# Kernel optimization log

Measured on AMD Instinct MI355X. Metric: run time of the kernel, lower is better.

The kernel has to match this reference:

```python
import jax, jax.numpy as jnp
import numpy as np

N_NODES = 50000
N_EDGES = 600000
D_IN = 128
HIDDEN = 128
N_CLASSES = 2
BN_EPS = 1e-5


def setup_inputs() -> dict:
    key = jax.random.key(0)
    ks = jax.random.split(key, 10)
    x = jax.random.normal(ks[0], (N_NODES, D_IN), dtype=jnp.float32)
    edge_index = jax.random.randint(ks[1], (2, N_EDGES), 0, N_NODES, dtype=jnp.int64)
    # weights stored [in, out] (transpose of torch Linear.weight)
    s1 = 1.0 / np.sqrt(D_IN)
    s2 = 1.0 / np.sqrt(HIDDEN)
    W1 = jax.random.uniform(ks[2], (D_IN, HIDDEN), jnp.float32, -s1, s1)
    b1 = jax.random.uniform(ks[3], (HIDDEN,), jnp.float32, -s1, s1)
    gamma = jnp.ones((HIDDEN,), jnp.float32)
    beta = jnp.zeros((HIDDEN,), jnp.float32)
    W2 = jax.random.uniform(ks[4], (HIDDEN, HIDDEN), jnp.float32, -s2, s2)
    b2 = jax.random.uniform(ks[5], (HIDDEN,), jnp.float32, -s2, s2)
    Wl = jax.random.uniform(ks[6], (HIDDEN, N_CLASSES), jnp.float32, -s2, s2)
    bl = jax.random.uniform(ks[7], (N_CLASSES,), jnp.float32, -s2, s2)
    return {"x": x, "edge_index": edge_index, "W1": W1, "b1": b1,
            "gamma": gamma, "beta": beta, "W2": W2, "b2": b2,
            "Wl": Wl, "bl": bl}


def reference(x, edge_index, W1, b1, gamma, beta, W2, b2, Wl, bl):
    src, dst = edge_index[0], edge_index[1]
    # GINConv with eps=0 (PyG default): h_i = MLP(x_i + sum_{j->i} x_j)
    agg = jax.ops.segment_sum(x[src], dst, num_segments=N_NODES)  # [N, D]
    h = x + agg
    # MLP: Linear -> ReLU -> BatchNorm1d (train-mode batch stats) -> Linear
    h = jax.nn.relu(h @ W1 + b1)
    mean = jnp.mean(h, axis=0)
    var = jnp.var(h, axis=0)
    h = (h - mean) * jax.lax.rsqrt(var + BN_EPS) * gamma + beta
    h = h @ W2 + b2
    # classifier head
    return h @ Wl + bl  # [N, num_classes]
```

## Files before the change

kernel.cpp:

```cpp
#include <hip/hip_runtime.h>
#include <cstdint>

#define NN 50000
#define NE 600000
#define D 128
#define NWAVE 3125
#define NBLK 782
#define BS 48
#define NB 196
#define PCAP 4608
#define FA 147
#define WB1 16
#define XB4 782
#define NREP 16

typedef __attribute__((ext_vector_type(8))) short short8;
typedef __attribute__((ext_vector_type(4))) float f32x4;

static __device__ __forceinline__ unsigned short f2bf(float f) {
  unsigned int u = __float_as_uint(f);
  unsigned int r = (u + 0x7FFFu + ((u >> 16) & 1u)) >> 16;
  return (unsigned short)r;
}

__global__ __launch_bounds__(256) void k_prep(const float* __restrict__ x,
                                              const float* __restrict__ W1,
                                              const float* __restrict__ W2,
                                              const float* __restrict__ Wl,
                                              const float* __restrict__ b2,
                                              const float* __restrict__ bl,
                                              const int* __restrict__ ei,
                                              unsigned short* __restrict__ xb,
                                              unsigned short* __restrict__ W1p,
                                              float* __restrict__ Cf,
                                              float* __restrict__ KBf,
                                              int* __restrict__ gcnt,
                                              unsigned* __restrict__ pairs) {
  __shared__ int histA[NB], baseA[NB], curA[NB];
  int blk = blockIdx.x, t = threadIdx.x;
  if (blk < FA) {
    if (t < NB) histA[t] = 0;
    __syncthreads();
    int e0 = blk * 4096 + t;
#pragma unroll
    for (int i = 0; i < 16; ++i) {
      int e = e0 + i * 256;
      if (e < NE) atomicAdd(&histA[ei[NE + e] >> 8], 1);
    }
    __syncthreads();
    if (t < NB) {
      int h = histA[t];
      baseA[t] = h ? atomicAdd(&gcnt[t], h) : 0;
      curA[t] = 0;
    }
    __syncthreads();
#pragma unroll
    for (int i = 0; i < 16; ++i) {
      int e = e0 + i * 256;
      if (e < NE) {
        int s = ei[e];
        int d = ei[NE + e];
        int b = d >> 8;
        int p = baseA[b] + atomicAdd(&curA[b], 1);
        if (p < PCAP) pairs[b * PCAP + p] = (unsigned)s | ((unsigned)(d & 255) << 16);
      }
    }
    return;
  }
  blk -= FA;
  if (blk < WB1) {
    int base = blk * 1024 + t;
#pragma unroll
    for (int i = 0; i < 4; ++i) {
      int rem = base + i * 256;
      int ks = rem >> 12;
      int nf = (rem >> 9) & 7;
      int l  = (rem >> 3) & 63;
      int j  = rem & 7;
      int k = ks * 32 + (l >> 4) * 8 + j;
      int n = nf * 16 + (l & 15);
      W1p[rem] = f2bf(W1[k * D + n]);
    }
    return;
  }
  blk -= WB1;
  if (blk == 0) {
    {
      int k = t >> 1, c = t & 1;
      const float4* w2r = (const float4*)(W2 + k * D);
      float s = 0.f;
#pragma unroll
      for (int m4 = 0; m4 < 32; ++m4) {
        float4 wv = w2r[m4];
        int m = m4 * 4;
        s += wv.x * Wl[(m + 0) * 2 + c] + wv.y * Wl[(m + 1) * 2 + c] +
             wv.z * Wl[(m + 2) * 2 + c] + wv.w * Wl[(m + 3) * 2 + c];
      }
      Cf[k * 2 + c] = s;
    }
    if (t < 2) {
      float s = bl[t];
      for (int m = 0; m < D; ++m) s += b2[m] * Wl[m * 2 + t];
      KBf[t] = s;
    }
    return;
  }
  blk -= 1;
  {
    int64_t base = (int64_t)blk * 1024 + t;
    const float4* xs = (const float4*)x;
#pragma unroll
    for (int i = 0; i < 4; ++i) {
      int64_t idx = base + i * 256;
      if (idx < (int64_t)NN * D / 8) {
        float4 f0 = xs[idx * 2], f1 = xs[idx * 2 + 1];
        uint4 o;
        o.x = (unsigned)f2bf(f0.x) | ((unsigned)f2bf(f0.y) << 16);
        o.y = (unsigned)f2bf(f0.z) | ((unsigned)f2bf(f0.w) << 16);
        o.z = (unsigned)f2bf(f1.x) | ((unsigned)f2bf(f1.y) << 16);
        o.w = (unsigned)f2bf(f1.z) | ((unsigned)f2bf(f1.w) << 16);
        ((uint4*)xb)[idx] = o;
      }
    }
  }
}

__global__ __launch_bounds__(256) void k_fusedA(const unsigned short* __restrict__ xb,
                                                const int* __restrict__ gcnt,
                                                const unsigned* __restrict__ pairs,
                                                const unsigned short* __restrict__ W1p,
                                                const float* __restrict__ b1,
                                                unsigned short* __restrict__ h1b,
                                                float* __restrict__ stats) {
  __shared__ uint4 tile[64 * 16];
  __shared__ unsigned short cs[64 * BS];
  __shared__ int cur[64];
  __shared__ float redS[D], redQ[D];
  int t = threadIdx.x;
  if (t < D) { redS[t] = 0.f; redQ[t] = 0.f; }
  if (t < 64) cur[t] = 0;
  __syncthreads();

  {
    int bkt = blockIdx.x >> 2, qt = blockIdx.x & 3;
    int cnt = gcnt[bkt]; if (cnt > PCAP) cnt = PCAP;
    for (int i = t; i < cnt; i += 256) {
      unsigned u = pairs[bkt * PCAP + i];
      int dloc = (u >> 16) & 255;
      if ((dloc >> 6) == qt) {
        int dl = dloc & 63;
        int pos = atomicAdd(&cur[dl], 1);
        if (pos < BS - 1) cs[dl * BS + pos] = (unsigned short)(u & 0xFFFFu);
      }
    }
  }
  __syncthreads();

  int w = t >> 6, lane = t & 63;
  int g = lane >> 4, l = lane & 15;
  int wave_id = blockIdx.x * 4 + w;
  bool valid = wave_id < NWAVE;
  int row0 = wave_id * 16;
  const uint4* xv = (const uint4*)xb;

  if (valid) {
#define GSRC(k) __shfl(((k) < 16 ? cl0 : ((k) < 32 ? cl1 : cl2)), (g << 4) + ((k) & 15))
#define MSK(v, kk) { unsigned m_ = ((kk) < dcap) ? 0xFFFFFFFFu : 0u; \
                     (v).x &= m_; (v).y &= m_; (v).z &= m_; (v).w &= m_; }
#define ACC8(v)                                     \
  { a0 += __uint_as_float((v).x << 16);             \
    a1 += __uint_as_float((v).x & 0xFFFF0000u);     \
    a2 += __uint_as_float((v).y << 16);             \
    a3 += __uint_as_float((v).y & 0xFFFF0000u);     \
    a4 += __uint_as_float((v).z << 16);             \
    a5 += __uint_as_float((v).z & 0xFFFF0000u);     \
    a6 += __uint_as_float((v).w << 16);             \
    a7 += __uint_as_float((v).w & 0xFFFF0000u); }
    for (int sub = 0; sub < 4; ++sub) {
      int dl = (w << 4) + (sub << 2) + g;
      int node = blockIdx.x * 64 + dl;
      int ec = cur[dl];
      if (ec > BS - 1) ec = BS - 1;
      int dcap = ec + 1;
      int cbase = dl * BS;
      int cl0 = (l < ec) ? (int)cs[cbase + l]
                         : ((l == ec) ? node : 0);
      int cl1 = (l + 16 < ec) ? (int)cs[cbase + 16 + l]
                              : ((l + 16 == ec) ? node : 0);
      int cl2 = (l + 32 < ec) ? (int)cs[cbase + 32 + l]
                              : ((l + 32 == ec) ? node : 0);
      int maxd = dcap;
      maxd = max(maxd, __shfl_xor(maxd, 16));
      maxd = max(maxd, __shfl_xor(maxd, 32));
      float a0 = 0, a1 = 0, a2 = 0, a3 = 0, a4 = 0, a5 = 0, a6 = 0, a7 = 0;
      int nit = (maxd + 7) >> 3;
      for (int it = 0; it < nit; ++it) {
        int k0 = it << 3;
        int i0 = GSRC(k0);
        int i1 = GSRC(k0 + 1);
        int i2 = GSRC(k0 + 2);
        int i3 = GSRC(k0 + 3);
        int i4 = GSRC(k0 + 4);
        int i5 = GSRC(k0 + 5);
        int i6 = GSRC(k0 + 6);
        int i7 = GSRC(k0 + 7);
        uint4 v0 = xv[(unsigned)i0 * 16u + l];
        uint4 v1 = xv[(unsigned)i1 * 16u + l];
        uint4 v2 = xv[(unsigned)i2 * 16u + l];
        uint4 v3 = xv[(unsigned)i3 * 16u + l];
        uint4 v4 = xv[(unsigned)i4 * 16u + l];
        uint4 v5 = xv[(unsigned)i5 * 16u + l];
        uint4 v6 = xv[(unsigned)i6 * 16u + l];
        uint4 v7 = xv[(unsigned)i7 * 16u + l];
        MSK(v0, k0) MSK(v1, k0 + 1) MSK(v2, k0 + 2) MSK(v3, k0 + 3)
        MSK(v4, k0 + 4) MSK(v5, k0 + 5) MSK(v6, k0 + 6) MSK(v7, k0 + 7)
        ACC8(v0) ACC8(v1) ACC8(v2) ACC8(v3)
        ACC8(v4) ACC8(v5) ACC8(v6) ACC8(v7)
      }
      uint4 o;
      o.x = (unsigned)f2bf(a0) | ((unsigned)f2bf(a1) << 16);
      o.y = (unsigned)f2bf(a2) | ((unsigned)f2bf(a3) << 16);
      o.z = (unsigned)f2bf(a4) | ((unsigned)f2bf(a5) << 16);
      o.w = (unsigned)f2bf(a6) | ((unsigned)f2bf(a7) << 16);
      tile[(dl * 16 + l) ^ (dl & 7)] = o;
    }
#undef GSRC
#undef MSK
#undef ACC8

    {
      int rb = (w << 4) + l;
      short8 a[4];
#pragma unroll
      for (int ks = 0; ks < 4; ++ks)
        a[ks] = *(const short8*)&tile[(rb * 16 + ks * 4 + g) ^ (rb & 7)];

      f32x4 acc[8];
#pragma unroll
      for (int nf = 0; nf < 8; ++nf) { f32x4 z = {0.f, 0.f, 0.f, 0.f}; acc[nf] = z; }

      const short8* B = (const short8*)W1p;
#pragma unroll
      for (int ks = 0; ks < 4; ++ks)
#pragma unroll
        for (int nf = 0; nf < 8; ++nf)
          acc[nf] = __builtin_amdgcn_mfma_f32_16x16x32_bf16(a[ks], B[(ks * 8 + nf) * 64 + lane],
                                                            acc[nf], 0, 0, 0);

#pragma unroll
      for (int nf = 0; nf < 8; ++nf) {
        int colc = nf * 16 + l;
        float bias = b1[colc];
        float ps = 0.f, pq = 0.f;
#pragma unroll
        for (int r = 0; r < 4; ++r) {
          float v = fmaxf(acc[nf][r] + bias, 0.f);
          int row = row0 + g * 4 + r;
          h1b[(int64_t)row * D + colc] = f2bf(v);
          ps += v; pq += v * v;
        }
        ps += __shfl_xor(ps, 16); ps += __shfl_xor(ps, 32);
        pq += __shfl_xor(pq, 16); pq += __shfl_xor(pq, 32);
        if (g == 0) { atomicAdd(&redS[colc], ps); atomicAdd(&redQ[colc], pq); }
      }
    }
  }
  __syncthreads();
  {
    int r = blockIdx.x & (NREP - 1);
    if (t < D) {
      unsafeAtomicAdd(&stats[r * 256 + t], redS[t]);
      unsafeAtomicAdd(&stats[r * 256 + D + t], redQ[t]);
    }
  }
}

__global__ __launch_bounds__(256) void k_head(const unsigned short* __restrict__ h1b,
                                              const float* __restrict__ stats,
                                              const float* __restrict__ gamma,
                                              const float* __restrict__ beta,
                                              const float* __restrict__ Cf,
                                              const float* __restrict__ KBf,
                                              float* __restrict__ out) {
  __shared__ float sc_s[D], sh_s[D];
  __shared__ float2 c2_s[D];
  int t = threadIdx.x;
  if (t < D) {
    float s = 0.f, q = 0.f;
#pragma unroll
    for (int r = 0; r < NREP; ++r) {
      s += stats[r * 256 + t];
      q += stats[r * 256 + D + t];
    }
    const float inv_n = 1.0f / (float)NN;
    float mean = s * inv_n;
    float var = q * inv_n - mean * mean;
    float sc = gamma[t] * rsqrtf(var + 1e-5f);
    sc_s[t] = sc;
    sh_s[t] = beta[t] - mean * sc;
    c2_s[t] = ((const float2*)Cf)[t];
  }
  __syncthreads();
  float2 kb = ((const float2*)KBf)[0];
  int l = t & 15;
  int k0 = l * 8;
#pragma unroll
  for (int rd = 0; rd < 4; ++rd) {
    int node = blockIdx.x * 64 + rd * 16 + (t >> 4);
    if (node < NN) {
      uint4 v = ((const uint4*)h1b)[(int64_t)node * 16 + l];
      float e0 = __uint_as_float(v.x << 16), e1 = __uint_as_float(v.x & 0xFFFF0000u);
      float e2 = __uint_as_float(v.y << 16), e3 = __uint_as_float(v.y & 0xFFFF0000u);
      float e4 = __uint_as_float(v.z << 16), e5 = __uint_as_float(v.z & 0xFFFF0000u);
      float e6 = __uint_as_float(v.w << 16), e7 = __uint_as_float(v.w & 0xFFFF0000u);
      float p0 = 0.f, p1 = 0.f;
#define HC(ej, jj) { float u_ = ej * sc_s[k0 + jj] + sh_s[k0 + jj];  \
                     float2 c_ = c2_s[k0 + jj];                      \
                     p0 += u_ * c_.x; p1 += u_ * c_.y; }
      HC(e0, 0) HC(e1, 1) HC(e2, 2) HC(e3, 3) HC(e4, 4) HC(e5, 5) HC(e6, 6) HC(e7, 7)
#undef HC
      p0 += __shfl_xor(p0, 1); p0 += __shfl_xor(p0, 2);
      p0 += __shfl_xor(p0, 4); p0 += __shfl_xor(p0, 8);
      p1 += __shfl_xor(p1, 1); p1 += __shfl_xor(p1, 2);
      p1 += __shfl_xor(p1, 4); p1 += __shfl_xor(p1, 8);
      if (l == 0) ((float2*)out)[node] = make_float2(p0 + kb.x, p1 + kb.y);
    }
  }
}

extern "C" void kernel_launch(void* const* d_in, const int* in_sizes, int n_in,
                              void* d_out, int out_size, void* d_ws, size_t ws_size,
                              hipStream_t stream) {
  const float* x     = (const float*)d_in[0];
  const int*   ei    = (const int*)d_in[1];
  const float* W1    = (const float*)d_in[2];
  const float* b1    = (const float*)d_in[3];
  const float* gamma = (const float*)d_in[4];
  const float* beta  = (const float*)d_in[5];
  const float* W2    = (const float*)d_in[6];
  const float* b2    = (const float*)d_in[7];
  const float* Wl    = (const float*)d_in[8];
  const float* bl    = (const float*)d_in[9];
  float* out = (float*)d_out;

  unsigned short* xb  = (unsigned short*)d_ws;
  unsigned short* h1b = xb + (int64_t)NN * D;
  unsigned short* W1p = h1b + (int64_t)NN * D;
  float* Cf     = (float*)(W1p + 16384);
  float* KBf    = Cf + 256;
  float* stats  = KBf + 4;
  int* gcnt     = (int*)(stats + NREP * 256);
  unsigned* pairs = (unsigned*)(gcnt + 256);

  hipMemsetAsync(stats, 0, (NREP * 256 + 256) * sizeof(float), stream);
  k_prep<<<FA + WB1 + 1 + XB4, 256, 0, stream>>>(x, W1, W2, Wl, b2, bl, ei,
                                                 xb, W1p, Cf, KBf, gcnt, pairs);
  k_fusedA<<<NBLK, 256, 0, stream>>>(xb, gcnt, pairs, W1p, b1, h1b, stats);
  k_head<<<NBLK, 256, 0, stream>>>(h1b, stats, gamma, beta, Cf, KBf, out);
}
```

Before: 73.33 us.

## Shrink destination buckets to 32 nodes and double block count for aggregation

Edge buckets now cover 32 destination nodes instead of 256, so each fused aggregation block reads only its own bucket rather than scanning a 256-node bucket and discarding three quarters of the entries. Blocks handle 32 nodes, which doubles the grid for the aggregation and head kernels. The MFMA stage is split so that each wave computes half the output columns for 16 rows. The prep kernel keeps edge indices in registers instead of reading them twice. In exchange there are more global histogram atomics over 1563 buckets, a larger shared histogram, and a smaller per-bucket capacity (640) that could overflow on skewed graphs.

```diff
diff --git a/kernel.cpp b/kernel.cpp
--- a/kernel.cpp
+++ b/kernel.cpp
@@ -4,11 +4,9 @@
 #define NN 50000
 #define NE 600000
 #define D 128
-#define NWAVE 3125
-#define NBLK 782
 #define BS 48
-#define NB 196
-#define PCAP 4608
+#define NB2 1563
+#define PCAP2 640
 #define FA 147
 #define WB1 16
 #define XB4 782
@@ -36,33 +34,35 @@
                                               float* __restrict__ KBf,
                                               int* __restrict__ gcnt,
                                               unsigned* __restrict__ pairs) {
-  __shared__ int histA[NB], baseA[NB], curA[NB];
+  __shared__ int histA[NB2], baseA[NB2], curA[NB2];
   int blk = blockIdx.x, t = threadIdx.x;
   if (blk < FA) {
-    if (t < NB) histA[t] = 0;
+    for (int i = t; i < NB2; i += 256) histA[i] = 0;
     __syncthreads();
     int e0 = blk * 4096 + t;
+    int sreg[16], dreg[16];
 #pragma unroll
     for (int i = 0; i < 16; ++i) {
       int e = e0 + i * 256;
-      if (e < NE) atomicAdd(&histA[ei[NE + e] >> 8], 1);
+      bool ok = e < NE;
+      sreg[i] = ok ? ei[e] : 0;
+      dreg[i] = ok ? ei[NE + e] : -1;
+      if (ok) atomicAdd(&histA[dreg[i] >> 5], 1);
     }
     __syncthreads();
-    if (t < NB) {
-      int h = histA[t];
-      baseA[t] = h ? atomicAdd(&gcnt[t], h) : 0;
-      curA[t] = 0;
+    for (int i = t; i < NB2; i += 256) {
+      int h = histA[i];
+      baseA[i] = h ? atomicAdd(&gcnt[i], h) : 0;
+      curA[i] = 0;
     }
     __syncthreads();
 #pragma unroll
     for (int i = 0; i < 16; ++i) {
-      int e = e0 + i * 256;
-      if (e < NE) {
-        int s = ei[e];
-        int d = ei[NE + e];
-        int b = d >> 8;
+      if (dreg[i] >= 0) {
+        int b = dreg[i] >> 5;
         int p = baseA[b] + atomicAdd(&curA[b], 1);
-        if (p < PCAP) pairs[b * PCAP + p] = (unsigned)s | ((unsigned)(d & 255) << 16);
+        if (p < PCAP2)
+          pairs[b * PCAP2 + p] = (unsigned)sreg[i] | ((unsigned)(dreg[i] & 31) << 16);
       }
     }
     return;
@@ -132,38 +132,30 @@
                                                 const float* __restrict__ b1,
                                                 unsigned short* __restrict__ h1b,
                                                 float* __restrict__ stats) {
-  __shared__ uint4 tile[64 * 16];
-  __shared__ unsigned short cs[64 * BS];
-  __shared__ int cur[64];
+  __shared__ uint4 tile[32 * 16];
+  __shared__ unsigned short cs[32 * BS];
+  __shared__ int cur[32];
   __shared__ float redS[D], redQ[D];
-  int t = threadIdx.x;
+  int t = threadIdx.x, b = blockIdx.x;
   if (t < D) { redS[t] = 0.f; redQ[t] = 0.f; }
-  if (t < 64) cur[t] = 0;
+  if (t < 32) cur[t] = 0;
   __syncthreads();
 
   {
-    int bkt = blockIdx.x >> 2, qt = blockIdx.x & 3;
-    int cnt = gcnt[bkt]; if (cnt > PCAP) cnt = PCAP;
+    int cnt = gcnt[b]; if (cnt > PCAP2) cnt = PCAP2;
     for (int i = t; i < cnt; i += 256) {
-      unsigned u = pairs[bkt * PCAP + i];
-      int dloc = (u >> 16) & 255;
-      if ((dloc >> 6) == qt) {
-        int dl = dloc & 63;
-        int pos = atomicAdd(&cur[dl], 1);
-        if (pos < BS - 1) cs[dl * BS + pos] = (unsigned short)(u & 0xFFFFu);
-      }
+      unsigned u = pairs[b * PCAP2 + i];
+      int dl = (u >> 16) & 31;
+      int pos = atomicAdd(&cur[dl], 1);
+      if (pos < BS - 1) cs[dl * BS + pos] = (unsigned short)(u & 0xFFFFu);
     }
   }
   __syncthreads();
 
   int w = t >> 6, lane = t & 63;
   int g = lane >> 4, l = lane & 15;
-  int wave_id = blockIdx.x * 4 + w;
-  bool valid = wave_id < NWAVE;
-  int row0 = wave_id * 16;
   const uint4* xv = (const uint4*)xb;
 
-  if (valid) {
 #define GSRC(k) __shfl(((k) < 16 ? cl0 : ((k) < 32 ? cl1 : cl2)), (g << 4) + ((k) & 15))
 #define MSK(v, kk) { unsigned m_ = ((kk) < dcap) ? 0xFFFFFFFFu : 0u; \
                      (v).x &= m_; (v).y &= m_; (v).z &= m_; (v).w &= m_; }
@@ -176,93 +168,99 @@
     a5 += __uint_as_float((v).z & 0xFFFF0000u);     \
     a6 += __uint_as_float((v).w << 16);             \
     a7 += __uint_as_float((v).w & 0xFFFF0000u); }
-    for (int sub = 0; sub < 4; ++sub) {
-      int dl = (w << 4) + (sub << 2) + g;
-      int node = blockIdx.x * 64 + dl;
-      int ec = cur[dl];
-      if (ec > BS - 1) ec = BS - 1;
-      int dcap = ec + 1;
-      int cbase = dl * BS;
-      int cl0 = (l < ec) ? (int)cs[cbase + l]
-                         : ((l == ec) ? node : 0);
-      int cl1 = (l + 16 < ec) ? (int)cs[cbase + 16 + l]
-                              : ((l + 16 == ec) ? node : 0);
-      int cl2 = (l + 32 < ec) ? (int)cs[cbase + 32 + l]
-                              : ((l + 32 == ec) ? node : 0);
-      int maxd = dcap;
-      maxd = max(maxd, __shfl_xor(maxd, 16));
-      maxd = max(maxd, __shfl_xor(maxd, 32));
-      float a0 = 0, a1 = 0, a2 = 0, a3 = 0, a4 = 0, a5 = 0, a6 = 0, a7 = 0;
-      int nit = (maxd + 7) >> 3;
-      for (int it = 0; it < nit; ++it) {
-        int k0 = it << 3;
-        int i0 = GSRC(k0);
-        int i1 = GSRC(k0 + 1);
-        int i2 = GSRC(k0 + 2);
-        int i3 = GSRC(k0 + 3);
-        int i4 = GSRC(k0 + 4);
-        int i5 = GSRC(k0 + 5);
-        int i6 = GSRC(k0 + 6);
-        int i7 = GSRC(k0 + 7);
-        uint4 v0 = xv[(unsigned)i0 * 16u + l];
-        uint4 v1 = xv[(unsigned)i1 * 16u + l];
-        uint4 v2 = xv[(unsigned)i2 * 16u + l];
-        uint4 v3 = xv[(unsigned)i3 * 16u + l];
-        uint4 v4 = xv[(unsigned)i4 * 16u + l];
-        uint4 v5 = xv[(unsigned)i5 * 16u + l];
-        uint4 v6 = xv[(unsigned)i6 * 16u + l];
-        uint4 v7 = xv[(unsigned)i7 * 16u + l];
-        MSK(v0, k0) MSK(v1, k0 + 1) MSK(v2, k0 + 2) MSK(v3, k0 + 3)
-        MSK(v4, k0 + 4) MSK(v5, k0 + 5) MSK(v6, k0 + 6) MSK(v7, k0 + 7)
-        ACC8(v0) ACC8(v1) ACC8(v2) ACC8(v3)
-        ACC8(v4) ACC8(v5) ACC8(v6) ACC8(v7)
-      }
-      uint4 o;
-      o.x = (unsigned)f2bf(a0) | ((unsigned)f2bf(a1) << 16);
-      o.y = (unsigned)f2bf(a2) | ((unsigned)f2bf(a3) << 16);
-      o.z = (unsigned)f2bf(a4) | ((unsigned)f2bf(a5) << 16);
-      o.w = (unsigned)f2bf(a6) | ((unsigned)f2bf(a7) << 16);
-      tile[(dl * 16 + l) ^ (dl & 7)] = o;
-    }
+  for (int sub = 0; sub < 2; ++sub) {
+    int dl = (w << 3) + (sub << 2) + g;
+    int node = b * 32 + dl;
+    int ec = cur[dl];
+    if (ec > BS - 1) ec = BS - 1;
+    int dcap = ec + 1;
+    int selfn = (node < NN) ? node : 0;
+    int cbase = dl * BS;
+    int cl0 = (l < ec) ? (int)cs[cbase + l]
+                       : ((l == ec) ? selfn : 0);
+    int cl1 = (l + 16 < ec) ? (int)cs[cbase + 16 + l]
+                            : ((l + 16 == ec) ? selfn : 0);
+    int cl2 = (l + 32 < ec) ? (int)cs[cbase + 32 + l]
+                            : ((l + 32 == ec) ? selfn : 0);
+    int maxd = dcap;
+    maxd = max(maxd, __shfl_xor(maxd, 16));
+    maxd = max(maxd, __shfl_xor(maxd, 32));
+    float a0 = 0, a1 = 0, a2 = 0, a3 = 0, a4 = 0, a5 = 0, a6 = 0, a7 = 0;
+    int nit = (maxd + 7) >> 3;
+    for (int it = 0; it < nit; ++it) {
+      int k0 = it << 3;
+      int i0 = GSRC(k0);
+      int i1 = GSRC(k0 + 1);
+      int i2 = GSRC(k0 + 2);
+      int i3 = GSRC(k0 + 3);
+      int i4 = GSRC(k0 + 4);
+      int i5 = GSRC(k0 + 5);
+      int i6 = GSRC(k0 + 6);
+      int i7 = GSRC(k0 + 7);
+      uint4 v0 = xv[(unsigned)i0 * 16u + l];
+      uint4 v1 = xv[(unsigned)i1 * 16u + l];
+      uint4 v2 = xv[(unsigned)i2 * 16u + l];
+      uint4 v3 = xv[(unsigned)i3 * 16u + l];
+      uint4 v4 = xv[(unsigned)i4 * 16u + l];
+      uint4 v5 = xv[(unsigned)i5 * 16u + l];
+      uint4 v6 = xv[(unsigned)i6 * 16u + l];
+      uint4 v7 = xv[(unsigned)i7 * 16u + l];
+      MSK(v0, k0) MSK(v1, k0 + 1) MSK(v2, k0 + 2) MSK(v3, k0 + 3)
+      MSK(v4, k0 + 4) MSK(v5, k0 + 5) MSK(v6, k0 + 6) MSK(v7, k0 + 7)
+      ACC8(v0) ACC8(v1) ACC8(v2) ACC8(v3)
+      ACC8(v4) ACC8(v5) ACC8(v6) ACC8(v7)
+    }
+    uint4 o;
+    o.x = (unsigned)f2bf(a0) | ((unsigned)f2bf(a1) << 16);
+    o.y = (unsigned)f2bf(a2) | ((unsigned)f2bf(a3) << 16);
+    o.z = (unsigned)f2bf(a4) | ((unsigned)f2bf(a5) << 16);
+    o.w = (unsigned)f2bf(a6) | ((unsigned)f2bf(a7) << 16);
+    tile[(dl * 16 + l) ^ (dl & 7)] = o;
+  }
 #undef GSRC
 #undef MSK
 #undef ACC8
-
-    {
-      int rb = (w << 4) + l;
-      short8 a[4];
-#pragma unroll
-      for (int ks = 0; ks < 4; ++ks)
-        a[ks] = *(const short8*)&tile[(rb * 16 + ks * 4 + g) ^ (rb & 7)];
-
-      f32x4 acc[8];
-#pragma unroll
-      for (int nf = 0; nf < 8; ++nf) { f32x4 z = {0.f, 0.f, 0.f, 0.f}; acc[nf] = z; }
-
-      const short8* B = (const short8*)W1p;
-#pragma unroll
-      for (int ks = 0; ks < 4; ++ks)
-#pragma unroll
-        for (int nf = 0; nf < 8; ++nf)
-          acc[nf] = __builtin_amdgcn_mfma_f32_16x16x32_bf16(a[ks], B[(ks * 8 + nf) * 64 + lane],
-                                                            acc[nf], 0, 0, 0);
-
-#pragma unroll
-      for (int nf = 0; nf < 8; ++nf) {
-        int colc = nf * 16 + l;
-        float bias = b1[colc];
-        float ps = 0.f, pq = 0.f;
-#pragma unroll
-        for (int r = 0; r < 4; ++r) {
-          float v = fmaxf(acc[nf][r] + bias, 0.f);
-          int row = row0 + g * 4 + r;
+  __syncthreads();
+
+  {
+    int th = w >> 1, nh = w & 1;
+    int rbt = th * 16 + l;
+    short8 a[4];
+#pragma unroll
+    for (int ks = 0; ks < 4; ++ks)
+      a[ks] = *(const short8*)&tile[(rbt * 16 + ks * 4 + g) ^ (rbt & 7)];
+
+    f32x4 acc[4];
+#pragma unroll
+    for (int nfl = 0; nfl < 4; ++nfl) { f32x4 z = {0.f, 0.f, 0.f, 0.f}; acc[nfl] = z; }
+
+    const short8* B = (const short8*)W1p;
+#pragma unroll
+    for (int ks = 0; ks < 4; ++ks)
+#pragma unroll
+      for (int nfl = 0; nfl < 4; ++nfl) {
+        int nf = nh * 4 + nfl;
+        acc[nfl] = __builtin_amdgcn_mfma_f32_16x16x32_bf16(a[ks], B[(ks * 8 + nf) * 64 + lane],
+                                                           acc[nfl], 0, 0, 0);
+      }
+
+#pragma unroll
+    for (int nfl = 0; nfl < 4; ++nfl) {
+      int colc = (nh * 4 + nfl) * 16 + l;
+      float bias = b1[colc];
+      float ps = 0.f, pq = 0.f;
+#pragma unroll
+      for (int r = 0; r < 4; ++r) {
+        int row = b * 32 + th * 16 + g * 4 + r;
+        float v = fmaxf(acc[nfl][r] + bias, 0.f);
+        if (row < NN) {
           h1b[(int64_t)row * D + colc] = f2bf(v);
           ps += v; pq += v * v;
         }
-        ps += __shfl_xor(ps, 16); ps += __shfl_xor(ps, 32);
-        pq += __shfl_xor(pq, 16); pq += __shfl_xor(pq, 32);
-        if (g == 0) { atomicAdd(&redS[colc], ps); atomicAdd(&redQ[colc], pq); }
-      }
+      }
+      ps += __shfl_xor(ps, 16); ps += __shfl_xor(ps, 32);
+      pq += __shfl_xor(pq, 16); pq += __shfl_xor(pq, 32);
+      if (g == 0) { atomicAdd(&redS[colc], ps); atomicAdd(&redQ[colc], pq); }
     }
   }
   __syncthreads();
@@ -305,8 +303,8 @@
   int l = t & 15;
   int k0 = l * 8;
 #pragma unroll
-  for (int rd = 0; rd < 4; ++rd) {
-    int node = blockIdx.x * 64 + rd * 16 + (t >> 4);
+  for (int rd = 0; rd < 2; ++rd) {
+    int node = blockIdx.x * 32 + rd * 16 + (t >> 4);
     if (node < NN) {
       uint4 v = ((const uint4*)h1b)[(int64_t)node * 16 + l];
       float e0 = __uint_as_float(v.x << 16), e1 = __uint_as_float(v.x & 0xFFFF0000u);
@@ -350,11 +348,11 @@
   float* KBf    = Cf + 256;
   float* stats  = KBf + 4;
   int* gcnt     = (int*)(stats + NREP * 256);
-  unsigned* pairs = (unsigned*)(gcnt + 256);
-
-  hipMemsetAsync(stats, 0, (NREP * 256 + 256) * sizeof(float), stream);
+  unsigned* pairs = (unsigned*)(gcnt + NB2);
+
+  hipMemsetAsync(stats, 0, (NREP * 256 + NB2) * sizeof(float), stream);
   k_prep<<<FA + WB1 + 1 + XB4, 256, 0, stream>>>(x, W1, W2, Wl, b2, bl, ei,
                                                  xb, W1p, Cf, KBf, gcnt, pairs);
-  k_fusedA<<<NBLK, 256, 0, stream>>>(xb, gcnt, pairs, W1p, b1, h1b, stats);
-  k_head<<<NBLK, 256, 0, stream>>>(h1b, stats, gamma, beta, Cf, KBf, out);
-}
+  k_fusedA<<<NB2, 256, 0, stream>>>(xb, gcnt, pairs, W1p, b1, h1b, stats);
+  k_head<<<NB2, 256, 0, stream>>>(h1b, stats, gamma, beta, Cf, KBf, out);
+}
```

Measured after the change: 70.59 us (median of 2 runs). -3.7%, faster.
